# Kernel tuning notes

Hardware: AMD Instinct MI355X
Metric: run time of the kernel (lower is better)

## Reference

```python
import jax, jax.numpy as jnp
import numpy as np

H = 8          # query heads
KVH = 1        # key/value heads
HD = 256       # head dim
ROPE_BASE = 10000.0


def _rotate_half(x):
    x1, x2 = x[..., : HD // 2], x[..., HD // 2 :]
    return jnp.concatenate((-x2, x1), axis=-1)


def _rope_cos_sin(position_ids):
    # position_ids: [B, S] int -> cos/sin: [B, S, HD]
    inv_freq = 1.0 / (ROPE_BASE ** (jnp.arange(0, HD, 2, dtype=jnp.float32) / HD))
    freqs = position_ids.astype(jnp.float32)[..., None] * inv_freq  # [B,S,HD/2]
    emb = jnp.concatenate((freqs, freqs), axis=-1)                  # [B,S,HD]
    return jnp.cos(emb), jnp.sin(emb)


def setup_inputs() -> dict:
    key = jax.random.key(0)
    ks = jax.random.split(key, 5)
    B, S, D = 2, 2048, 2048
    return {
        "hidden_states": jax.random.normal(ks[0], (B, S, D), dtype=jnp.float32),
        "attention_mask": jnp.zeros((B, 1, S, S), dtype=jnp.float32),
        "position_ids": jnp.broadcast_to(jnp.arange(S, dtype=jnp.int32), (B, S)),
        "Wq": jax.random.normal(ks[1], (D, H * HD), dtype=jnp.float32) * 0.02,
        "Wk": jax.random.normal(ks[2], (D, KVH * HD), dtype=jnp.float32) * 0.02,
        "Wv": jax.random.normal(ks[3], (D, KVH * HD), dtype=jnp.float32) * 0.02,
        "Wo": jax.random.normal(ks[4], (H * HD, D), dtype=jnp.float32) * 0.02,
    }


def reference(hidden_states, attention_mask, position_ids, Wq, Wk, Wv, Wo):
    B, S, D = hidden_states.shape
    # projections -> [B, heads, S, HD]
    q = jnp.einsum("bsd,df->bsf", hidden_states, Wq).reshape(B, S, H, HD).transpose(0, 2, 1, 3)
    k = jnp.einsum("bsd,df->bsf", hidden_states, Wk).reshape(B, S, KVH, HD).transpose(0, 2, 1, 3)
    v = jnp.einsum("bsd,df->bsf", hidden_states, Wv).reshape(B, S, KVH, HD).transpose(0, 2, 1, 3)

    cos, sin = _rope_cos_sin(position_ids)
    cos, sin = cos[:, None], sin[:, None]  # unsqueeze head dim
    q = q * cos + _rotate_half(q) * sin
    k = k * cos + _rotate_half(k) * sin

    # GQA: repeat kv heads to match query heads
    rep = H // KVH
    k = jnp.repeat(k, rep, axis=1)
    v = jnp.repeat(v, rep, axis=1)

    d_k = D // H  # matches torch code's scaling (== HD here)
    scores = jnp.einsum("bhqd,bhkd->bhqk", q, k) / jnp.sqrt(jnp.float32(d_k))
    scores = scores + attention_mask
    attn = jax.nn.softmax(scores, axis=-1)  # dropout p=0 / eval mode

    out = jnp.einsum("bhqk,bhkd->bhqd", attn, v)  # [B,H,S,HD]
    out = out.transpose(0, 2, 1, 3).reshape(B, S, H * HD)
    out = jnp.einsum("bsf,fd->bsd", out, Wo)
    return out
```

## Files before the change

### kernel.cpp

```cpp
#include <hip/hip_runtime.h>
#include <cmath>


typedef __bf16 bf16;
typedef __attribute__((ext_vector_type(8))) __bf16 bf16x8;
typedef __attribute__((ext_vector_type(4))) __bf16 bf16x4;
typedef __attribute__((ext_vector_type(4))) float f32x4;

#define S_LEN 2048
#define D_MODEL 2048
#define H_NUM 8
#define HDIM 256
#define NT (S_LEN / 64)
#define SM_BIAS 8.0f

__device__ __forceinline__ void gl_lds16(const bf16* g, bf16* l) {
  __builtin_amdgcn_global_load_lds(
      (const __attribute__((address_space(1))) void*)g,
      (__attribute__((address_space(3))) void*)l, 16, 0, 0);
}

__global__ void cvt_bf16(const float* __restrict__ src, bf16* __restrict__ dst) {
  const int i = (blockIdx.x * 256 + threadIdx.x) * 4;
  const float4 v = *(const float4*)(src + i);
  bf16x4 o;
  o[0] = (bf16)v.x; o[1] = (bf16)v.y; o[2] = (bf16)v.z; o[3] = (bf16)v.w;
  *(bf16x4*)(dst + i) = o;
}

__global__ void tpose_all(const float* __restrict__ Wq, const float* __restrict__ Wk,
                          const float* __restrict__ Wv, const float* __restrict__ Wo,
                          bf16* __restrict__ Wqkvt, bf16* __restrict__ Wot) {
  __shared__ float t[32][33];
  const int tx = threadIdx.x, ty = threadIdx.y;
  const int bx = blockIdx.x;
  const int k0 = blockIdx.y * 32;
  const float* W; bf16* Wt; int Ncols, no0, n0;
  if (bx < 64)      { W = Wq; Wt = Wqkvt; Ncols = 2048; no0 = 0;    n0 = bx * 32; }
  else if (bx < 72) { W = Wk; Wt = Wqkvt; Ncols = 256;  no0 = 2048; n0 = (bx - 64) * 32; }
  else if (bx < 80) { W = Wv; Wt = Wqkvt; Ncols = 256;  no0 = 2304; n0 = (bx - 72) * 32; }
  else              { W = Wo; Wt = Wot;   Ncols = 2048; no0 = 0;    n0 = (bx - 80) * 32; }
#pragma unroll
  for (int i = 0; i < 4; ++i)
    t[ty + 8 * i][tx] = W[(size_t)(k0 + ty + 8 * i) * Ncols + (n0 + tx)];
  __syncthreads();
#pragma unroll
  for (int i = 0; i < 4; ++i)
    Wt[(size_t)(no0 + n0 + ty + 8 * i) * D_MODEL + (k0 + tx)] = (bf16)t[tx][ty + 8 * i];
}

__global__ __launch_bounds__(256)
void gemm_bf16(const bf16* __restrict__ A, const bf16* __restrict__ Wt,
               bf16* __restrict__ Cq, bf16* __restrict__ Ck, bf16* __restrict__ Cv,
               float* __restrict__ Cf, int M, int N, int mode) {
  __shared__ bf16 As[128 * 32];
  __shared__ bf16 Bs[128 * 32];
  const int tid = threadIdx.x;
  const int lane = tid & 63;
  const int wbase = tid & 192;
  const int c16 = lane & 15;
  const int quad = lane >> 4;
  const int wave = tid >> 6;
  const int wr = wave >> 1, wc = wave & 1;
  const int m0 = blockIdx.y * 128, n0 = blockIdx.x * 128;

  f32x4 acc[4][4];
#pragma unroll
  for (int i = 0; i < 4; ++i)
#pragma unroll
    for (int j = 0; j < 4; ++j)
#pragma unroll
      for (int r = 0; r < 4; ++r) acc[i][j][r] = 0.f;

  for (int k0 = 0; k0 < D_MODEL; k0 += 32) {
#pragma unroll
    for (int j = 0; j < 2; ++j) {
      const int bslot = j * 256 + wbase;
      const int slot = bslot + lane;
      const int row = slot >> 2, ch = slot & 3;
      gl_lds16(&A[(size_t)(m0 + row) * D_MODEL + k0 + ch * 8], &As[bslot * 8]);
      gl_lds16(&Wt[(size_t)(n0 + row) * D_MODEL + k0 + ch * 8], &Bs[bslot * 8]);
    }
    __syncthreads();
    bf16x8 af[4], bfr[4];
#pragma unroll
    for (int i = 0; i < 4; ++i)
      af[i] = *(const bf16x8*)&As[(wr * 64 + i * 16 + c16) * 32 + quad * 8];
#pragma unroll
    for (int j = 0; j < 4; ++j)
      bfr[j] = *(const bf16x8*)&Bs[(wc * 64 + j * 16 + c16) * 32 + quad * 8];
#pragma unroll
    for (int i = 0; i < 4; ++i)
#pragma unroll
      for (int j = 0; j < 4; ++j)
        acc[i][j] = __builtin_amdgcn_mfma_f32_16x16x32_bf16(af[i], bfr[j], acc[i][j], 0, 0, 0);
    __syncthreads();
  }

#pragma unroll
  for (int i = 0; i < 4; ++i)
#pragma unroll
    for (int j = 0; j < 4; ++j) {
      const int n = n0 + wc * 64 + j * 16 + c16;
#pragma unroll
      for (int r = 0; r < 4; ++r) {
        const int m = m0 + wr * 64 + i * 16 + quad * 4 + r;
        const float val = acc[i][j][r];
        if (mode == 1) {
          const int b = m >> 11, s = m & 2047;
          if (n0 < 2048) {
            const int h = n >> 8, hd = n & 255;
            Cq[((((size_t)b * H_NUM + h) * S_LEN + s) << 8) + hd] = (bf16)val;
          } else if (n0 < 2304) {
            Ck[((size_t)m << 8) + (n - 2048)] = (bf16)val;
          } else {
            Cv[((size_t)((b << 8) + (n - 2304)) << 11) + s] = (bf16)val;
          }
        } else {
          Cf[(size_t)m * D_MODEL + n] = val;
        }
      }
    }
}

#define ROPE_C (-0.07195578415606394f)

__global__ void rope_all(bf16* __restrict__ q, bf16* __restrict__ k,
                         const int* __restrict__ pos, int BHS) {
  const int idx = blockIdx.x * 256 + threadIdx.x;
  const int j = idx & 127;
  const int t = idx >> 7;
  float sn, cs;
  if (t < BHS) {
    const int s = t & 2047;
    const int b = t >> 14;
    const float p = (float)pos[(b << 11) + s];
    sincosf(p * expf((float)j * ROPE_C), &sn, &cs);
    bf16* base = q + ((size_t)t << 8);
    const float x1 = (float)base[j], x2 = (float)base[j + 128];
    base[j] = (bf16)(x1 * cs - x2 * sn);
    base[j + 128] = (bf16)(x2 * cs + x1 * sn);
  } else {
    const int t2 = t - BHS;
    const int s = t2 & 2047;
    const int b = t2 >> 11;
    const float p = (float)pos[(b << 11) + s];
    sincosf(p * expf((float)j * ROPE_C), &sn, &cs);
    bf16* base = k + ((size_t)t2 << 8);
    const float x1 = (float)base[j], x2 = (float)base[j + 128];
    base[j] = (bf16)(x1 * cs - x2 * sn);
    base[j + 128] = (bf16)(x2 * cs + x1 * sn);
  }
}

__global__ __launch_bounds__(512, 2)
void flash_bf16(const bf16* __restrict__ qg, const bf16* __restrict__ kg,
                const bf16* __restrict__ vg, const float* __restrict__ msk,
                bf16* __restrict__ ao) {
  __shared__ bf16 Ks[2][64 * 256];
  __shared__ bf16 Vs[2][256 * 64];
  __shared__ bf16 Ps[128 * 64];
  __shared__ float Lp[2][128];

  const int tid = threadIdx.x;
  const int lane = tid & 63;
  const int w = tid >> 6;
  const int c16 = lane & 15;
  const int quad = lane >> 4;
  const int qi = w & 3;
  const int sec = w >> 2;

  const int bidx = blockIdx.x;
  int b, qb;
  if (gridDim.x == 256) {
    b = (bidx & 7) >> 2;
    qb = ((bidx & 3) << 5) | (bidx >> 3);
  } else {
    b = bidx >> 7;
    qb = bidx & 127;
  }
  const int q0 = qb * 16;

  const bf16* qh = qg + ((((size_t)b * H_NUM + qi * 2) * S_LEN + q0) << 8);
  const char* kbase = (const char*)(kg + ((size_t)b << 19));
  const char* vbase = (const char*)(vg + ((size_t)b << 19));
  const float* mbase = msk + (size_t)b * S_LEN * S_LEN + (size_t)q0 * S_LEN;

  bf16x8 qf[2][8];
#pragma unroll
  for (int mi = 0; mi < 2; ++mi)
#pragma unroll
    for (int kd = 0; kd < 8; ++kd)
      qf[mi][kd] = *(const bf16x8*)&qh[(((size_t)mi * S_LEN + c16) << 8) + kd * 32 + quad * 8];

  f32x4 oacc[2][8];
#pragma unroll
  for (int mi = 0; mi < 2; ++mi)
#pragma unroll
    for (int nj = 0; nj < 8; ++nj)
#pragma unroll
      for (int r = 0; r < 4; ++r) oacc[mi][nj][r] = 0.f;
  float plsum[2][4];
#pragma unroll
  for (int mi = 0; mi < 2; ++mi)
#pragma unroll
    for (int r = 0; r < 4; ++r) plsum[mi][r] = 0.f;

  auto stage = [&](int k0, int buf) {
#pragma unroll
    for (int j = 0; j < 4; ++j) {
      const int ki = w * 4 + j;
      const int krow = ki * 2 + (lane >> 5);
      const int kcb = ((lane & 31) * 16) ^ ((krow & 7) << 4);
      gl_lds16((const bf16*)(kbase + ((size_t)(k0 + krow) << 9) + kcb),
               &Ks[buf][ki * 512]);
      const int vrow = ki * 8 + (lane >> 3);
      const int vcb = ((lane & 7) * 16) ^ ((vrow & 7) << 4);
      gl_lds16((const bf16*)(vbase + ((size_t)vrow << 12) + (k0 << 1) + vcb),
               &Vs[buf][ki * 512]);
    }
  };

  stage(0, 0);
  __syncthreads();

  for (int t = 0; t < NT; ++t) {
    const int k0 = t * 64;
    const int buf = t & 1;
    if (t + 1 < NT) stage(k0 + 64, buf ^ 1);

    float ml[2][4];
#pragma unroll
    for (int nj = 0; nj < 2; ++nj)
#pragma unroll
      for (int r = 0; r < 4; ++r)
        ml[nj][r] = mbase[(size_t)(quad * 4 + r) * S_LEN +
                          k0 + sec * 32 + nj * 16 + c16];

    f32x4 sc[2][2];
#pragma unroll
    for (int mi = 0; mi < 2; ++mi)
#pragma unroll
      for (int nj = 0; nj < 2; ++nj)
#pragma unroll
        for (int r = 0; r < 4; ++r) sc[mi][nj][r] = 0.f;
    __builtin_amdgcn_s_setprio(1);
#pragma unroll
    for (int kd = 0; kd < 8; ++kd) {
      bf16x8 bK[2];
#pragma unroll
      for (int nj = 0; nj < 2; ++nj) {
        const int row = sec * 32 + nj * 16 + c16;
        bK[nj] = *(const bf16x8*)((const char*)&Ks[buf][0] + row * 512 +
                                  ((kd * 64 + quad * 16) ^ ((row & 7) << 4)));
      }
#pragma unroll
      for (int mi = 0; mi < 2; ++mi)
#pragma unroll
        for (int nj = 0; nj < 2; ++nj)
          sc[mi][nj] = __builtin_amdgcn_mfma_f32_16x16x32_bf16(qf[mi][kd], bK[nj], sc[mi][nj], 0, 0, 0);
    }
    __builtin_amdgcn_s_setprio(0);

#pragma unroll
    for (int mi = 0; mi < 2; ++mi)
#pragma unroll
      for (int nj = 0; nj < 2; ++nj)
#pragma unroll
        for (int r = 0; r < 4; ++r) {
          const float p = __expf(sc[mi][nj][r] * 0.0625f + ml[nj][r] - SM_BIAS);
          plsum[mi][r] += p;
          const int row = qi * 32 + mi * 16 + quad * 4 + r;
          const int cb = ((sec * 32 + nj * 16 + c16) * 2) ^ ((row & 7) << 4);
          *(bf16*)((char*)&Ps[0] + row * 128 + cb) = (bf16)p;
        }

    __builtin_amdgcn_sched_barrier(0);
    asm volatile("s_waitcnt lgkmcnt(0)" ::: "memory");
    __builtin_amdgcn_s_barrier();
    __builtin_amdgcn_sched_barrier(0);

    bf16x8 pa[2][2];
#pragma unroll
    for (int mi = 0; mi < 2; ++mi)
#pragma unroll
      for (int ks = 0; ks < 2; ++ks) {
        const int row = qi * 32 + mi * 16 + c16;
        pa[mi][ks] = *(const bf16x8*)((const char*)&Ps[0] + row * 128 +
                                      ((ks * 64 + quad * 16) ^ ((row & 7) << 4)));
      }
    __builtin_amdgcn_s_setprio(1);
#pragma unroll
    for (int nj = 0; nj < 8; ++nj) {
#pragma unroll
      for (int ks = 0; ks < 2; ++ks) {
        const int drow = sec * 128 + nj * 16 + c16;
        const bf16x8 bv = *(const bf16x8*)((const char*)&Vs[buf][0] + drow * 128 +
                                           ((ks * 64 + quad * 16) ^ ((drow & 7) << 4)));
#pragma unroll
        for (int mi = 0; mi < 2; ++mi)
          oacc[mi][nj] = __builtin_amdgcn_mfma_f32_16x16x32_bf16(pa[mi][ks], bv, oacc[mi][nj], 0, 0, 0);
      }
    }
    __builtin_amdgcn_s_setprio(0);

    __syncthreads();
  }

#pragma unroll
  for (int mi = 0; mi < 2; ++mi)
#pragma unroll
    for (int r = 0; r < 4; ++r) {
      float s = plsum[mi][r];
      s += __shfl_xor(s, 1, 64);
      s += __shfl_xor(s, 2, 64);
      s += __shfl_xor(s, 4, 64);
      s += __shfl_xor(s, 8, 64);
      if (c16 == 0) Lp[sec][qi * 32 + mi * 16 + quad * 4 + r] = s;
    }
  __syncthreads();
  float li[2][4];
#pragma unroll
  for (int mi = 0; mi < 2; ++mi)
#pragma unroll
    for (int r = 0; r < 4; ++r) {
      const int row = qi * 32 + mi * 16 + quad * 4 + r;
      li[mi][r] = 1.f / (Lp[0][row] + Lp[1][row]);
    }
  bf16* obase = ao + (size_t)(b * S_LEN + q0 + quad * 4) * D_MODEL + qi * 512 + sec * 128;
#pragma unroll
  for (int mi = 0; mi < 2; ++mi)
#pragma unroll
    for (int nj = 0; nj < 8; ++nj)
#pragma unroll
      for (int r = 0; r < 4; ++r)
        obase[(size_t)r * D_MODEL + mi * 256 + nj * 16 + c16] =
            (bf16)(oacc[mi][nj][r] * li[mi][r]);
}

extern "C" void kernel_launch(void* const* d_in, const int* in_sizes, int n_in,
                              void* d_out, int out_size, void* d_ws, size_t ws_size,
                              hipStream_t stream) {
  const float* hs   = (const float*)d_in[0];
  const float* mask = (const float*)d_in[1];
  const int*   pos  = (const int*)d_in[2];
  const float* Wq   = (const float*)d_in[3];
  const float* Wk   = (const float*)d_in[4];
  const float* Wv   = (const float*)d_in[5];
  const float* Wo   = (const float*)d_in[6];
  float* out = (float*)d_out;

  const int B = in_sizes[2] / S_LEN;
  const int M = B * S_LEN;

  char* wsc = (char*)d_ws;
  bf16* hsb = (bf16*)wsc;
  bf16* aob = hsb;
  size_t off = (size_t)M * D_MODEL * 2;
  bf16* Wqkvt = (bf16*)(wsc + off); off += (size_t)2560 * D_MODEL * 2;
  bf16* Wot   = (bf16*)(wsc + off); off += (size_t)D_MODEL * D_MODEL * 2;
  bf16* kb    = (bf16*)(wsc + off);
  bf16* vb    = kb + (size_t)M * HDIM;

  bf16* qb = (bf16*)d_out;

  const dim3 blk(256);
  cvt_bf16<<<(M * D_MODEL) / 1024, blk, 0, stream>>>(hs, hsb);
  tpose_all<<<dim3(144, 64), dim3(32, 8), 0, stream>>>(Wq, Wk, Wv, Wo, Wqkvt, Wot);

  gemm_bf16<<<dim3(20, M / 128), blk, 0, stream>>>(hsb, Wqkvt, qb, kb, vb, nullptr, M, 2560, 1);

  rope_all<<<(B * (H_NUM + 1) * S_LEN * 128) / 256, blk, 0, stream>>>(
      qb, kb, pos, B * H_NUM * S_LEN);

  flash_bf16<<<B * (S_LEN / 16), dim3(512), 0, stream>>>(qb, kb, vb, mask, aob);

  gemm_bf16<<<dim3(16, M / 128), blk, 0, stream>>>(aob, Wot, nullptr, nullptr, nullptr, out, M, D_MODEL, 3);
}
```

Measured before the change: 398.5 us.

## Rewrite GEMM as 256x256 tiled, double-buffered, swizzled-LDS 8-wave pipeline

Replaces the 128x128, single-buffered GEMM with a 512-thread kernel computing 256x256 tiles over 64-wide K chunks. Global-to-LDS loads are double-buffered and interleaved with MFMA quadrants, with explicit vmcnt waits and barriers. LDS uses an XOR swizzle to avoid bank conflicts, and workgroups are remapped across XCDs. This raises data reuse and overlaps memory with compute for the QKV and output projections, at the cost of more LDS, more registers and fewer blocks (tile quantization).

```diff
diff --git a/kernel.cpp b/kernel.cpp
--- a/kernel.cpp
+++ b/kernel.cpp
@@ -13,6 +13,8 @@
 #define HDIM 256
 #define NT (S_LEN / 64)
 #define SM_BIAS 8.0f
+
+#define BAR __builtin_amdgcn_s_barrier()
 
 __device__ __forceinline__ void gl_lds16(const bf16* g, bf16* l) {
   __builtin_amdgcn_global_load_lds(
@@ -49,62 +51,133 @@
     Wt[(size_t)(no0 + n0 + ty + 8 * i) * D_MODEL + (k0 + tx)] = (bf16)t[tx][ty + 8 * i];
 }
 
-__global__ __launch_bounds__(256)
+__global__ __launch_bounds__(512, 2)
 void gemm_bf16(const bf16* __restrict__ A, const bf16* __restrict__ Wt,
                bf16* __restrict__ Cq, bf16* __restrict__ Ck, bf16* __restrict__ Cv,
-               float* __restrict__ Cf, int M, int N, int mode) {
-  __shared__ bf16 As[128 * 32];
-  __shared__ bf16 Bs[128 * 32];
+               float* __restrict__ Cf, int NX, int mode) {
+  __shared__ bf16 As[2][2][128 * 64];
+  __shared__ bf16 Bs[2][2][128 * 64];
   const int tid = threadIdx.x;
   const int lane = tid & 63;
-  const int wbase = tid & 192;
+  const int w = tid >> 6;
   const int c16 = lane & 15;
   const int quad = lane >> 4;
-  const int wave = tid >> 6;
-  const int wr = wave >> 1, wc = wave & 1;
-  const int m0 = blockIdx.y * 128, n0 = blockIdx.x * 128;
-
-  f32x4 acc[4][4];
-#pragma unroll
-  for (int i = 0; i < 4; ++i)
+  const int wm = w >> 2;
+  const int wn = w & 3;
+
+  const int nwg = gridDim.x;
+  const int swz = (blockIdx.x & 7) * (nwg >> 3) + (blockIdx.x >> 3);
+  const int m0 = (swz / NX) * 256;
+  const int n0 = (swz % NX) * 256;
+
+  const char* Ab = (const char*)A;
+  const char* Bb = (const char*)Wt;
+  const int lr8 = lane >> 3;
+  const int scb = ((lane & 7) ^ lr8) << 4;
+
+  f32x4 acc[8][4];
+#pragma unroll
+  for (int i = 0; i < 8; ++i)
 #pragma unroll
     for (int j = 0; j < 4; ++j)
 #pragma unroll
       for (int r = 0; r < 4; ++r) acc[i][j][r] = 0.f;
 
-  for (int k0 = 0; k0 < D_MODEL; k0 += 32) {
+  auto stg = [&](const char* gcol, int grow0, bf16* lhalf) {
+#pragma unroll
+    for (int j2 = 0; j2 < 2; ++j2) {
+      const int c = w * 2 + j2;
+      gl_lds16((const bf16*)(gcol + (size_t)(grow0 + c * 8 + lr8) * 4096 + scb),
+               lhalf + c * 512);
+    }
+  };
+  auto ldA = [&](int sl, int qm, bf16x8* d) {
+    const char* base = (const char*)&As[sl][wm][0];
+#pragma unroll
+    for (int i = 0; i < 4; ++i) {
+      const int row = qm * 64 + i * 16 + c16;
+      const int sw = (row & 7) << 4;
+#pragma unroll
+      for (int kk = 0; kk < 2; ++kk)
+        d[i * 2 + kk] = *(const bf16x8*)(base + row * 128 + ((kk * 64 + quad * 16) ^ sw));
+    }
+  };
+  auto ldB = [&](int sl, int qn, bf16x8* d) {
+    const char* base = (const char*)&Bs[sl][wn >> 1][0];
 #pragma unroll
     for (int j = 0; j < 2; ++j) {
-      const int bslot = j * 256 + wbase;
-      const int slot = bslot + lane;
-      const int row = slot >> 2, ch = slot & 3;
-      gl_lds16(&A[(size_t)(m0 + row) * D_MODEL + k0 + ch * 8], &As[bslot * 8]);
-      gl_lds16(&Wt[(size_t)(n0 + row) * D_MODEL + k0 + ch * 8], &Bs[bslot * 8]);
-    }
-    __syncthreads();
-    bf16x8 af[4], bfr[4];
-#pragma unroll
-    for (int i = 0; i < 4; ++i)
-      af[i] = *(const bf16x8*)&As[(wr * 64 + i * 16 + c16) * 32 + quad * 8];
-#pragma unroll
-    for (int j = 0; j < 4; ++j)
-      bfr[j] = *(const bf16x8*)&Bs[(wc * 64 + j * 16 + c16) * 32 + quad * 8];
-#pragma unroll
-    for (int i = 0; i < 4; ++i)
-#pragma unroll
-      for (int j = 0; j < 4; ++j)
-        acc[i][j] = __builtin_amdgcn_mfma_f32_16x16x32_bf16(af[i], bfr[j], acc[i][j], 0, 0, 0);
-    __syncthreads();
+      const int row = (wn & 1) * 64 + qn * 32 + j * 16 + c16;
+      const int sw = (row & 7) << 4;
+#pragma unroll
+      for (int kk = 0; kk < 2; ++kk)
+        d[j * 2 + kk] = *(const bf16x8*)(base + row * 128 + ((kk * 64 + quad * 16) ^ sw));
+    }
+  };
+  auto mm = [&](int qm, int qn, const bf16x8* a, const bf16x8* bb) {
+    __builtin_amdgcn_s_setprio(1);
+#pragma unroll
+    for (int kk = 0; kk < 2; ++kk)
+#pragma unroll
+      for (int i = 0; i < 4; ++i)
+#pragma unroll
+        for (int j = 0; j < 2; ++j)
+          acc[qm * 4 + i][qn * 2 + j] = __builtin_amdgcn_mfma_f32_16x16x32_bf16(
+              a[i * 2 + kk], bb[j * 2 + kk], acc[qm * 4 + i][qn * 2 + j], 0, 0, 0);
+    __builtin_amdgcn_s_setprio(0);
+  };
+
+  bf16x8 Xa[8], Ya[8], Xb[4], Yb[4];
+
+  stg(Ab, m0, &As[0][0][0]);        stg(Ab, m0 + 128, &As[0][1][0]);
+  stg(Bb, n0, &Bs[0][0][0]);        stg(Bb, n0 + 128, &Bs[0][1][0]);
+  stg(Bb + 128, n0, &Bs[1][0][0]);  stg(Bb + 128, n0 + 128, &Bs[1][1][0]);
+  asm volatile("s_waitcnt vmcnt(4)" ::: "memory");
+  BAR;
+
+  for (int t = 0; t < 16; ++t) {
+    const int kc = t * 256;
+    const bool pf = (t < 15);
+    ldA(0, 0, Xa); ldB(0, 0, Xb);
+    stg(Ab + kc + 128, m0, &As[1][0][0]);
+    BAR; mm(0, 0, Xa, Xb); BAR;
+    ldB(0, 1, Yb);
+    stg(Ab + kc + 128, m0 + 128, &As[1][1][0]);
+    BAR; mm(0, 1, Xa, Yb); BAR;
+    ldA(0, 1, Ya);
+    if (pf) stg(Bb + kc + 256, n0, &Bs[0][0][0]);
+    BAR; mm(1, 1, Ya, Yb); BAR;
+    if (pf) stg(Bb + kc + 256, n0 + 128, &Bs[0][1][0]);
+    BAR; mm(1, 0, Ya, Xb);
+    if (pf) asm volatile("s_waitcnt vmcnt(4)" ::: "memory");
+    else    asm volatile("s_waitcnt vmcnt(0)" ::: "memory");
+    BAR;
+    ldA(1, 0, Xa); ldB(1, 0, Xb);
+    if (pf) stg(Ab + kc + 256, m0, &As[0][0][0]);
+    BAR; mm(0, 0, Xa, Xb); BAR;
+    ldB(1, 1, Yb);
+    if (pf) stg(Ab + kc + 256, m0 + 128, &As[0][1][0]);
+    BAR; mm(0, 1, Xa, Yb); BAR;
+    ldA(1, 1, Ya);
+    if (pf) stg(Bb + kc + 384, n0, &Bs[1][0][0]);
+    BAR; mm(1, 1, Ya, Yb); BAR;
+    if (pf) {
+      stg(Bb + kc + 384, n0 + 128, &Bs[1][1][0]);
+      BAR; mm(1, 0, Ya, Xb);
+      asm volatile("s_waitcnt vmcnt(4)" ::: "memory");
+      BAR;
+    } else {
+      BAR; mm(1, 0, Ya, Xb);
+    }
   }
 
 #pragma unroll
-  for (int i = 0; i < 4; ++i)
+  for (int i = 0; i < 8; ++i)
 #pragma unroll
     for (int j = 0; j < 4; ++j) {
-      const int n = n0 + wc * 64 + j * 16 + c16;
+      const int n = n0 + wn * 64 + j * 16 + c16;
 #pragma unroll
       for (int r = 0; r < 4; ++r) {
-        const int m = m0 + wr * 64 + i * 16 + quad * 4 + r;
+        const int m = m0 + wm * 128 + i * 16 + quad * 4 + r;
         const float val = acc[i][j][r];
         if (mode == 1) {
           const int b = m >> 11, s = m & 2047;
@@ -368,12 +441,12 @@
   cvt_bf16<<<(M * D_MODEL) / 1024, blk, 0, stream>>>(hs, hsb);
   tpose_all<<<dim3(144, 64), dim3(32, 8), 0, stream>>>(Wq, Wk, Wv, Wo, Wqkvt, Wot);
 
-  gemm_bf16<<<dim3(20, M / 128), blk, 0, stream>>>(hsb, Wqkvt, qb, kb, vb, nullptr, M, 2560, 1);
+  gemm_bf16<<<10 * (M / 256), dim3(512), 0, stream>>>(hsb, Wqkvt, qb, kb, vb, nullptr, 10, 1);
 
   rope_all<<<(B * (H_NUM + 1) * S_LEN * 128) / 256, blk, 0, stream>>>(
       qb, kb, pos, B * H_NUM * S_LEN);
 
   flash_bf16<<<B * (S_LEN / 16), dim3(512), 0, stream>>>(qb, kb, vb, mask, aob);
 
-  gemm_bf16<<<dim3(16, M / 128), blk, 0, stream>>>(aob, Wot, nullptr, nullptr, nullptr, out, M, D_MODEL, 3);
-}
+  gemm_bf16<<<8 * (M / 256), dim3(512), 0, stream>>>(aob, Wot, nullptr, nullptr, nullptr, out, 8, 3);
+}
```

Result: faster. 385.8 us (-3.2%).
